# Kernel tuning notes

Hardware: AMD Instinct MI355X
Metric: run time of the kernel (lower is better)

The kernel has to match this reference:

```python
import jax, jax.numpy as jnp
import numpy as np

ATTN_K = 64
H = 256  # seq_hidden_size


def setup_inputs() -> dict:
    key = jax.random.key(0)
    ks = jax.random.split(key, 10)
    N, Q = 1000000, 256
    return {
        "question": jax.random.normal(ks[0], (Q,), jnp.float32),
        "score": jax.random.uniform(ks[1], (), jnp.float32),
        "questions": jax.random.normal(ks[2], (N, Q), jnp.float32),
        "hs": jax.random.normal(ks[3], (N, H), jnp.float32),
        "W_score": jax.random.normal(ks[4], (1, Q + H), jnp.float32) * 0.05,
        "b_score": jax.random.normal(ks[5], (1,), jnp.float32) * 0.05,
        "W_ih": jax.random.normal(ks[6], (3 * H, 2 * Q), jnp.float32) * 0.05,
        "W_hh": jax.random.normal(ks[7], (3 * H, H), jnp.float32) * 0.05,
        "b_ih": jax.random.normal(ks[8], (3 * H,), jnp.float32) * 0.05,
        "b_hh": jax.random.normal(ks[9], (3 * H,), jnp.float32) * 0.05,
    }


def reference(question, score, questions, hs, W_score, b_score, W_ih, W_hh, b_ih, b_hh):
    # Attention over history: dot-product scores, top-k, softmax-weighted sum.
    alpha = questions @ question                      # [N]
    vals, idx = jax.lax.top_k(alpha, ATTN_K)          # [k], [k]
    w = jax.nn.softmax(vals)                          # softmax over the k selected scores
    attn_h = w @ hs[idx]                              # [H] weighted gather-sum

    # Score head on [question ; attn_h]
    pred_v = jnp.concatenate([question, attn_h])      # [Q+H]
    pred = W_score @ pred_v + b_score                 # [1]

    # GRU input: question gated by correctness of score
    right = (score >= 0.5).astype(question.dtype)
    x = jnp.concatenate([question * right, question * (1.0 - right)])  # [2Q]

    # Single GRU step (PyTorch gate ordering: r, z, n)
    h = hs[-1]                                        # [H]
    gx = W_ih @ x + b_ih                              # [3H]
    gh = W_hh @ h + b_hh                              # [3H]
    xr, xz, xn = gx[:H], gx[H:2 * H], gx[2 * H:]
    hr, hz, hn = gh[:H], gh[H:2 * H], gh[2 * H:]
    r = jax.nn.sigmoid(xr + hr)
    z = jax.nn.sigmoid(xz + hz)
    n = jnp.tanh(xn + r * hn)
    h_new = (1.0 - z) * n + z * h                     # [H]
    return pred, h_new
```

## Files before the change

### kernel.cpp

```cpp
#include <hip/hip_runtime.h>
#include <math.h>

#define Q 256
#define H 256
#define ATTN_K 64
#define CAP 4096
#define HBINS 4096

typedef float f4 __attribute__((ext_vector_type(4)));

__device__ __forceinline__ unsigned f2k(float f) {
    unsigned u = __float_as_uint(f);
    return u ^ ((u & 0x80000000u) ? 0xFFFFFFFFu : 0x80000000u);
}

__global__ __launch_bounds__(256) void k_main(const float* __restrict__ questions,
                                              const float* __restrict__ question,
                                              const float* __restrict__ score,
                                              const float* __restrict__ hs,
                                              const float* __restrict__ W_ih,
                                              const float* __restrict__ W_hh,
                                              const float* __restrict__ b_ih,
                                              const float* __restrict__ b_hh,
                                              float* __restrict__ gx, float* __restrict__ gh,
                                              unsigned* __restrict__ hist,
                                              unsigned* __restrict__ state,
                                              float* __restrict__ alpha, int N) {
    const int t = threadIdx.x;
    const int b = blockIdx.x;
    if (b < 16) hist[b * 256 + t] = 0u;
    if (b == 16 && t < 16) state[t] = 0u;

    const int lane = t & 63;
    const int wid = b * 4 + (t >> 6);

    if (wid < 3 * H) {
        const int o = wid;
        const int off = (score[0] >= 0.5f) ? 0 : Q;
        const float4 q = *reinterpret_cast<const float4*>(question + lane * 4);
        const float4 h = *reinterpret_cast<const float4*>(hs + (size_t)(N - 1) * H + lane * 4);
        const float4 wx = *reinterpret_cast<const float4*>(W_ih + (size_t)o * (2 * Q) + off + lane * 4);
        const float4 wh = *reinterpret_cast<const float4*>(W_hh + (size_t)o * H + lane * 4);
        float px = wx.x * q.x + wx.y * q.y + wx.z * q.z + wx.w * q.w;
        float ph = wh.x * h.x + wh.y * h.y + wh.z * h.z + wh.w * h.w;
#pragma unroll
        for (int d = 32; d > 0; d >>= 1) {
            px += __shfl_xor(px, d, 64);
            ph += __shfl_xor(ph, d, 64);
        }
        if (lane == 0) {
            gx[o] = px + b_ih[o];
            gh[o] = ph + b_hh[o];
        }
    }

    const int sub = lane & 15;
    const int rg  = lane >> 4;
    const int nw  = (gridDim.x * blockDim.x) >> 6;

    float4 q[4];
#pragma unroll
    for (int j = 0; j < 4; ++j)
        q[j] = *reinterpret_cast<const float4*>(question + j * 64 + sub * 4);

    const size_t stepRows = (size_t)nw * 8;
    const float* baseA = questions + (size_t)(wid * 8 + rg) * Q + sub * 4;
    for (size_t r0 = (size_t)wid * 8; r0 < (size_t)N; r0 += stepRows, baseA += stepRows * Q) {
        const int rA = (int)r0 + rg;
        const int rB = rA + 4;
        float pA = 0.f, pB = 0.f;
        if (rA < N) {
#pragma unroll
            for (int j = 0; j < 4; ++j) {
                f4 x = __builtin_nontemporal_load(reinterpret_cast<const f4*>(baseA + j * 64));
                pA = fmaf(x.x, q[j].x, fmaf(x.y, q[j].y, fmaf(x.z, q[j].z, fmaf(x.w, q[j].w, pA))));
            }
        }
        if (rB < N) {
#pragma unroll
            for (int j = 0; j < 4; ++j) {
                f4 x = __builtin_nontemporal_load(reinterpret_cast<const f4*>(baseA + 4 * Q + j * 64));
                pB = fmaf(x.x, q[j].x, fmaf(x.y, q[j].y, fmaf(x.z, q[j].z, fmaf(x.w, q[j].w, pB))));
            }
        }
#pragma unroll
        for (int d = 1; d < 16; d <<= 1) {
            pA += __shfl_xor(pA, d, 64);
            pB += __shfl_xor(pB, d, 64);
        }
        if (sub == 0) {
            if (rA < N) alpha[rA] = pA;
            if (rB < N) alpha[rB] = pB;
        }
    }
}

__global__ __launch_bounds__(1024) void k_histscan(const float* __restrict__ alpha,
                                                   unsigned* __restrict__ hist,
                                                   unsigned* __restrict__ state, int N) {
    __shared__ unsigned hb[HBINS];
    __shared__ unsigned wsum[16];
    __shared__ int flag_sh;
    const int t = threadIdx.x;
#pragma unroll
    for (int j = 0; j < HBINS / 1024; ++j) hb[t + j * 1024] = 0u;
    __syncthreads();

    const int n4 = N >> 2;
    const int stride = gridDim.x * blockDim.x;
    const float4* a4 = reinterpret_cast<const float4*>(alpha);
    for (int i = blockIdx.x * blockDim.x + t; i < n4; i += stride) {
        float4 a = a4[i];
        float v[4] = {a.x, a.y, a.z, a.w};
#pragma unroll
        for (int j = 0; j < 4; ++j) {
            int rel = (int)(f2k(v[j]) >> 19) - 4096;
            if (rel >= 0) atomicAdd(&hb[rel], 1u);
        }
    }
    if (blockIdx.x == 0 && t < (N & 3)) {
        float v = alpha[(n4 << 2) + t];
        int rel = (int)(f2k(v) >> 19) - 4096;
        if (rel >= 0) atomicAdd(&hb[rel], 1u);
    }
    __syncthreads();
#pragma unroll
    for (int j = 0; j < HBINS / 1024; ++j) {
        unsigned v = hb[t + j * 1024];
        if (v) atomicAdd(&hist[t + j * 1024], v);
    }

    if (t == 0) {
        __threadfence();
        unsigned a = atomicAdd(&state[3], 1u);
        flag_sh = (a == gridDim.x - 1) ? 1 : 0;
    }
    __syncthreads();
    if (!flag_sh) return;
    __threadfence();

    const uint4* h4 = reinterpret_cast<const uint4*>(hist);
    uint4 hv = h4[1023 - t];
    unsigned x = hv.x + hv.y + hv.z + hv.w;

    const int lane = t & 63;
    const int w = t >> 6;
#pragma unroll
    for (int d = 1; d < 64; d <<= 1) {
        unsigned y = __shfl_up(x, d, 64);
        if (lane >= d) x += y;
    }
    if (lane == 63) wsum[w] = x;
    __syncthreads();
    if (w == 0 && lane < 16) {
        unsigned s = wsum[lane];
#pragma unroll
        for (int d = 1; d < 16; d <<= 1) {
            unsigned y = __shfl_up(s, d, 64);
            if (lane >= d) s += y;
        }
        wsum[lane] = s;
    }
    __syncthreads();
    unsigned cum = x + ((w > 0) ? wsum[w - 1] : 0u);
    hb[t] = cum;
    __syncthreads();
    if (cum >= (unsigned)ATTN_K && (t == 0 || hb[t - 1] < (unsigned)ATTN_K)) {
        const int s = t;
        unsigned acc = (s > 0) ? hb[s - 1] : 0u;
        const int hi = 4095 - 4 * s;
        int tb = hi - 3;
        for (int bin = hi; bin >= hi - 3; --bin) {
            acc += hist[bin];
            if (acc >= (unsigned)ATTN_K) { tb = bin; break; }
        }
        state[0] = (unsigned)(tb + 4096);
    }
}

__global__ __launch_bounds__(256) void k_collecthead(const float* __restrict__ alpha,
                                                     const float* __restrict__ question,
                                                     const float* __restrict__ hs,
                                                     const float* __restrict__ W_score,
                                                     const float* __restrict__ b_score,
                                                     unsigned* __restrict__ state,
                                                     float* __restrict__ cval, int* __restrict__ cidx,
                                                     const float* __restrict__ gx,
                                                     const float* __restrict__ gh,
                                                     float* __restrict__ out, int N) {
    __shared__ float lv[CAP];
    __shared__ int li[CAP];
    __shared__ float sw[ATTN_K];
    __shared__ int si[ATTN_K];
    __shared__ float red[256];
    __shared__ int flag_sh;
    const int t = threadIdx.x;
    const int tau = (int)state[0];

    {
        const int stride = gridDim.x * blockDim.x;
        const int n4 = N >> 2;
        const float4* a4 = reinterpret_cast<const float4*>(alpha);
        for (int i = blockIdx.x * blockDim.x + t; i < n4; i += stride) {
            float4 a = a4[i];
            float v[4] = {a.x, a.y, a.z, a.w};
#pragma unroll
            for (int j = 0; j < 4; ++j) {
                if ((int)(f2k(v[j]) >> 19) >= tau) {
                    unsigned p = atomicAdd(&state[1], 1u);
                    if (p < CAP) { cval[p] = v[j]; cidx[p] = i * 4 + j; }
                }
            }
        }
        if (blockIdx.x == 0 && t < (N & 3)) {
            const int idx = (n4 << 2) + t;
            float v = alpha[idx];
            if ((int)(f2k(v) >> 19) >= tau) {
                unsigned p = atomicAdd(&state[1], 1u);
                if (p < CAP) { cval[p] = v; cidx[p] = idx; }
            }
        }
    }

    if (t == 0) {
        __threadfence();
        unsigned a = atomicAdd(&state[2], 1u);
        flag_sh = (a == gridDim.x - 1) ? 1 : 0;
    }
    __syncthreads();
    if (!flag_sh) return;
    __threadfence();

    const int C = min((int)state[1], CAP);
    for (int i = t; i < C; i += 256) { lv[i] = cval[i]; li[i] = cidx[i]; }
    __syncthreads();

    if (t < 64) {
        for (int k = 0; k < ATTN_K; ++k) {
            float bv = -INFINITY;
            int bi = 0x7fffffff;
            int bp = -1;
            for (int i = t; i < C; i += 64) {
                float v = lv[i];
                int id = li[i];
                if (v > bv || (v == bv && id < bi)) { bv = v; bi = id; bp = i; }
            }
#pragma unroll
            for (int d = 32; d > 0; d >>= 1) {
                float ov = __shfl_xor(bv, d, 64);
                int oi = __shfl_xor(bi, d, 64);
                int op = __shfl_xor(bp, d, 64);
                if (ov > bv || (ov == bv && oi < bi)) { bv = ov; bi = oi; bp = op; }
            }
            if (t == 0) {
                sw[k] = bv;
                si[k] = (bi == 0x7fffffff) ? 0 : bi;
                if (bp >= 0) lv[bp] = -INFINITY;
            }
        }
        float m = sw[0];
        float e = expf(sw[t] - m);
        float ssum = e;
#pragma unroll
        for (int d = 32; d > 0; d >>= 1) ssum += __shfl_xor(ssum, d, 64);
        sw[t] = e / ssum;
    }
    __syncthreads();

    float aj = 0.f;
    for (int k = 0; k < ATTN_K; ++k) {
        aj = fmaf(sw[k], hs[(size_t)si[k] * H + t], aj);
    }

    red[t] = W_score[t] * question[t] + W_score[Q + t] * aj;
    __syncthreads();
    for (int d = 128; d > 0; d >>= 1) {
        if (t < d) red[t] += red[t + d];
        __syncthreads();
    }
    if (t == 0) out[0] = red[0] + b_score[0];

    {
        float xr = gx[t], xz = gx[H + t], xn = gx[2 * H + t];
        float hr = gh[t], hz = gh[H + t], hn = gh[2 * H + t];
        float r = 1.f / (1.f + expf(-(xr + hr)));
        float z = 1.f / (1.f + expf(-(xz + hz)));
        float n = tanhf(xn + r * hn);
        float hprev = hs[(size_t)(N - 1) * H + t];
        out[1 + t] = (1.f - z) * n + z * hprev;
    }
}

extern "C" void kernel_launch(void* const* d_in, const int* in_sizes, int n_in,
                              void* d_out, int out_size, void* d_ws, size_t ws_size,
                              hipStream_t stream) {
    const float* question = (const float*)d_in[0];
    const float* score    = (const float*)d_in[1];
    const float* questions= (const float*)d_in[2];
    const float* hs       = (const float*)d_in[3];
    const float* W_score  = (const float*)d_in[4];
    const float* b_score  = (const float*)d_in[5];
    const float* W_ih     = (const float*)d_in[6];
    const float* W_hh     = (const float*)d_in[7];
    const float* b_ih     = (const float*)d_in[8];
    const float* b_hh     = (const float*)d_in[9];
    const int N = in_sizes[2] / Q;
    float* out = (float*)d_out;

    char* ws = (char*)d_ws;
    size_t off = 0;
    float* alpha = (float*)(ws + off); off += (size_t)N * sizeof(float);
    off = (off + 255) & ~(size_t)255;
    unsigned* hist = (unsigned*)(ws + off); off += (size_t)HBINS * sizeof(unsigned);
    unsigned* state = (unsigned*)(ws + off); off += 256;
    float* cval = (float*)(ws + off); off += (size_t)CAP * sizeof(float);
    int* cidx = (int*)(ws + off); off += (size_t)CAP * sizeof(int);
    float* gx = (float*)(ws + off); off += 3 * H * sizeof(float);
    float* gh = (float*)(ws + off); off += 3 * H * sizeof(float);

    k_main<<<2048, 256, 0, stream>>>(questions, question, score, hs, W_ih, W_hh,
                                     b_ih, b_hh, gx, gh, hist, state, alpha, N);
    k_histscan<<<64, 1024, 0, stream>>>(alpha, hist, state, N);
    k_collecthead<<<512, 256, 0, stream>>>(alpha, question, hs, W_score, b_score,
                                           state, cval, cidx, gx, gh, out, N);
}
```

Baseline: 238.3 us.

## Fuse histogram, threshold scan and candidate collection into one kernel

Merges the histogram/scan kernel and the collect/head kernel into a single kernel. Each thread holds its alpha values in registers across both phases, and the phases are separated by a grid-wide spin wait on a sentinel threshold published with release/acquire atomics. This removes one launch and the second pass over alpha. The main dot-product loop also loses its per-row bounds checks through a separate tail loop, and the weighted gather-sum is spread across 1024 threads. The spin wait relies on all 256 large blocks being co-resident, which risks deadlock if occupancy does not allow that.

```diff
diff --git a/kernel.cpp b/kernel.cpp
--- a/kernel.cpp
+++ b/kernel.cpp
@@ -6,6 +6,9 @@
 #define ATTN_K 64
 #define CAP 4096
 #define HBINS 4096
+#define SENTINEL 0xFFFFFFFFu
+#define SEL_BLOCKS 256
+#define SEL_THREADS 1024
 
 typedef float f4 __attribute__((ext_vector_type(4)));
 
@@ -29,7 +32,7 @@
     const int t = threadIdx.x;
     const int b = blockIdx.x;
     if (b < 16) hist[b * 256 + t] = 0u;
-    if (b == 16 && t < 16) state[t] = 0u;
+    if (b == 16 && t < 16) state[t] = (t == 0) ? SENTINEL : 0u;
 
     const int lane = t & 63;
     const int wid = b * 4 + (t >> 6);
@@ -63,25 +66,20 @@
     for (int j = 0; j < 4; ++j)
         q[j] = *reinterpret_cast<const float4*>(question + j * 64 + sub * 4);
 
+    const int B = N / (nw * 8);
     const size_t stepRows = (size_t)nw * 8;
-    const float* baseA = questions + (size_t)(wid * 8 + rg) * Q + sub * 4;
-    for (size_t r0 = (size_t)wid * 8; r0 < (size_t)N; r0 += stepRows, baseA += stepRows * Q) {
-        const int rA = (int)r0 + rg;
-        const int rB = rA + 4;
+    const float* baseA = questions + ((size_t)wid * 8 + rg) * Q + sub * 4;
+    for (int it = 0; it < B; ++it, baseA += stepRows * Q) {
         float pA = 0.f, pB = 0.f;
-        if (rA < N) {
-#pragma unroll
-            for (int j = 0; j < 4; ++j) {
-                f4 x = __builtin_nontemporal_load(reinterpret_cast<const f4*>(baseA + j * 64));
-                pA = fmaf(x.x, q[j].x, fmaf(x.y, q[j].y, fmaf(x.z, q[j].z, fmaf(x.w, q[j].w, pA))));
-            }
-        }
-        if (rB < N) {
-#pragma unroll
-            for (int j = 0; j < 4; ++j) {
-                f4 x = __builtin_nontemporal_load(reinterpret_cast<const f4*>(baseA + 4 * Q + j * 64));
-                pB = fmaf(x.x, q[j].x, fmaf(x.y, q[j].y, fmaf(x.z, q[j].z, fmaf(x.w, q[j].w, pB))));
-            }
+#pragma unroll
+        for (int j = 0; j < 4; ++j) {
+            f4 x = __builtin_nontemporal_load(reinterpret_cast<const f4*>(baseA + j * 64));
+            pA = fmaf(x.x, q[j].x, fmaf(x.y, q[j].y, fmaf(x.z, q[j].z, fmaf(x.w, q[j].w, pA))));
+        }
+#pragma unroll
+        for (int j = 0; j < 4; ++j) {
+            f4 x = __builtin_nontemporal_load(reinterpret_cast<const f4*>(baseA + 4 * Q + j * 64));
+            pB = fmaf(x.x, q[j].x, fmaf(x.y, q[j].y, fmaf(x.z, q[j].z, fmaf(x.w, q[j].w, pB))));
         }
 #pragma unroll
         for (int d = 1; d < 16; d <<= 1) {
@@ -89,150 +87,162 @@
             pB += __shfl_xor(pB, d, 64);
         }
         if (sub == 0) {
-            if (rA < N) alpha[rA] = pA;
-            if (rB < N) alpha[rB] = pB;
-        }
+            const size_t r0 = (size_t)it * stepRows + (size_t)wid * 8 + rg;
+            alpha[r0] = pA;
+            alpha[r0 + 4] = pB;
+        }
+    }
+
+    const int tailStart = B * nw * 8;
+    for (int g = wid; tailStart + g * 4 < N; g += nw) {
+        const int r = tailStart + g * 4 + rg;
+        float p = 0.f;
+        if (r < N) {
+            const float* row = questions + (size_t)r * Q + sub * 4;
+#pragma unroll
+            for (int j = 0; j < 4; ++j) {
+                f4 x = __builtin_nontemporal_load(reinterpret_cast<const f4*>(row + j * 64));
+                p = fmaf(x.x, q[j].x, fmaf(x.y, q[j].y, fmaf(x.z, q[j].z, fmaf(x.w, q[j].w, p))));
+            }
+        }
+#pragma unroll
+        for (int d = 1; d < 16; d <<= 1) p += __shfl_xor(p, d, 64);
+        if (sub == 0 && r < N) alpha[r] = p;
     }
 }
 
-__global__ __launch_bounds__(1024) void k_histscan(const float* __restrict__ alpha,
-                                                   unsigned* __restrict__ hist,
-                                                   unsigned* __restrict__ state, int N) {
+__global__ __launch_bounds__(SEL_THREADS) void k_select(const float* __restrict__ alpha,
+                                                        const float* __restrict__ question,
+                                                        const float* __restrict__ hs,
+                                                        const float* __restrict__ W_score,
+                                                        const float* __restrict__ b_score,
+                                                        unsigned* __restrict__ hist,
+                                                        unsigned* __restrict__ state,
+                                                        float* __restrict__ cval,
+                                                        int* __restrict__ cidx,
+                                                        const float* __restrict__ gx,
+                                                        const float* __restrict__ gh,
+                                                        float* __restrict__ out, int N) {
     __shared__ unsigned hb[HBINS];
-    __shared__ unsigned wsum[16];
-    __shared__ int flag_sh;
-    const int t = threadIdx.x;
-#pragma unroll
-    for (int j = 0; j < HBINS / 1024; ++j) hb[t + j * 1024] = 0u;
-    __syncthreads();
-
-    const int n4 = N >> 2;
-    const int stride = gridDim.x * blockDim.x;
-    const float4* a4 = reinterpret_cast<const float4*>(alpha);
-    for (int i = blockIdx.x * blockDim.x + t; i < n4; i += stride) {
-        float4 a = a4[i];
-        float v[4] = {a.x, a.y, a.z, a.w};
-#pragma unroll
-        for (int j = 0; j < 4; ++j) {
-            int rel = (int)(f2k(v[j]) >> 19) - 4096;
-            if (rel >= 0) atomicAdd(&hb[rel], 1u);
-        }
-    }
-    if (blockIdx.x == 0 && t < (N & 3)) {
-        float v = alpha[(n4 << 2) + t];
-        int rel = (int)(f2k(v) >> 19) - 4096;
-        if (rel >= 0) atomicAdd(&hb[rel], 1u);
-    }
-    __syncthreads();
-#pragma unroll
-    for (int j = 0; j < HBINS / 1024; ++j) {
-        unsigned v = hb[t + j * 1024];
-        if (v) atomicAdd(&hist[t + j * 1024], v);
-    }
-
-    if (t == 0) {
-        __threadfence();
-        unsigned a = atomicAdd(&state[3], 1u);
-        flag_sh = (a == gridDim.x - 1) ? 1 : 0;
-    }
-    __syncthreads();
-    if (!flag_sh) return;
-    __threadfence();
-
-    const uint4* h4 = reinterpret_cast<const uint4*>(hist);
-    uint4 hv = h4[1023 - t];
-    unsigned x = hv.x + hv.y + hv.z + hv.w;
-
-    const int lane = t & 63;
-    const int w = t >> 6;
-#pragma unroll
-    for (int d = 1; d < 64; d <<= 1) {
-        unsigned y = __shfl_up(x, d, 64);
-        if (lane >= d) x += y;
-    }
-    if (lane == 63) wsum[w] = x;
-    __syncthreads();
-    if (w == 0 && lane < 16) {
-        unsigned s = wsum[lane];
-#pragma unroll
-        for (int d = 1; d < 16; d <<= 1) {
-            unsigned y = __shfl_up(s, d, 64);
-            if (lane >= d) s += y;
-        }
-        wsum[lane] = s;
-    }
-    __syncthreads();
-    unsigned cum = x + ((w > 0) ? wsum[w - 1] : 0u);
-    hb[t] = cum;
-    __syncthreads();
-    if (cum >= (unsigned)ATTN_K && (t == 0 || hb[t - 1] < (unsigned)ATTN_K)) {
-        const int s = t;
-        unsigned acc = (s > 0) ? hb[s - 1] : 0u;
-        const int hi = 4095 - 4 * s;
-        int tb = hi - 3;
-        for (int bin = hi; bin >= hi - 3; --bin) {
-            acc += hist[bin];
-            if (acc >= (unsigned)ATTN_K) { tb = bin; break; }
-        }
-        state[0] = (unsigned)(tb + 4096);
-    }
-}
-
-__global__ __launch_bounds__(256) void k_collecthead(const float* __restrict__ alpha,
-                                                     const float* __restrict__ question,
-                                                     const float* __restrict__ hs,
-                                                     const float* __restrict__ W_score,
-                                                     const float* __restrict__ b_score,
-                                                     unsigned* __restrict__ state,
-                                                     float* __restrict__ cval, int* __restrict__ cidx,
-                                                     const float* __restrict__ gx,
-                                                     const float* __restrict__ gh,
-                                                     float* __restrict__ out, int N) {
     __shared__ float lv[CAP];
     __shared__ int li[CAP];
+    __shared__ float apart[4][256];
     __shared__ float sw[ATTN_K];
     __shared__ int si[ATTN_K];
     __shared__ float red[256];
-    __shared__ int flag_sh;
+    __shared__ unsigned wsum[16];
+    __shared__ int last_sh;
+    __shared__ unsigned tau_sh;
     const int t = threadIdx.x;
-    const int tau = (int)state[0];
+    const int gid = blockIdx.x * SEL_THREADS + t;
+    const int n4 = N >> 2;
+    const int span = SEL_BLOCKS * SEL_THREADS;
+
+    for (int j = t; j < HBINS; j += SEL_THREADS) hb[j] = 0u;
+    __syncthreads();
+
+    const float4* a4 = reinterpret_cast<const float4*>(alpha);
+    float4 a0 = make_float4(-1.f, -1.f, -1.f, -1.f);
+    float4 a1 = make_float4(-1.f, -1.f, -1.f, -1.f);
+    if (gid < n4) a0 = a4[gid];
+    if (gid + span < n4) a1 = a4[gid + span];
+    float rem = -1.f;
+    if (blockIdx.x == 0 && t < (N & 3)) rem = alpha[(n4 << 2) + t];
 
     {
-        const int stride = gridDim.x * blockDim.x;
-        const int n4 = N >> 2;
-        const float4* a4 = reinterpret_cast<const float4*>(alpha);
-        for (int i = blockIdx.x * blockDim.x + t; i < n4; i += stride) {
-            float4 a = a4[i];
-            float v[4] = {a.x, a.y, a.z, a.w};
-#pragma unroll
-            for (int j = 0; j < 4; ++j) {
-                if ((int)(f2k(v[j]) >> 19) >= tau) {
-                    unsigned p = atomicAdd(&state[1], 1u);
-                    if (p < CAP) { cval[p] = v[j]; cidx[p] = i * 4 + j; }
-                }
-            }
-        }
-        if (blockIdx.x == 0 && t < (N & 3)) {
-            const int idx = (n4 << 2) + t;
-            float v = alpha[idx];
-            if ((int)(f2k(v) >> 19) >= tau) {
-                unsigned p = atomicAdd(&state[1], 1u);
-                if (p < CAP) { cval[p] = v; cidx[p] = idx; }
-            }
-        }
+        float v[9] = {a0.x, a0.y, a0.z, a0.w, a1.x, a1.y, a1.z, a1.w, rem};
+#pragma unroll
+        for (int j = 0; j < 9; ++j) {
+            int rel = (int)(f2k(v[j]) >> 19) - 4096;
+            if (rel >= 0) atomicAdd(&hb[rel], 1u);
+        }
+    }
+    __syncthreads();
+    for (int j = t; j < HBINS; j += SEL_THREADS) {
+        unsigned v = hb[j];
+        if (v) atomicAdd(&hist[j], v);
     }
 
     if (t == 0) {
         __threadfence();
-        unsigned a = atomicAdd(&state[2], 1u);
-        flag_sh = (a == gridDim.x - 1) ? 1 : 0;
-    }
-    __syncthreads();
-    if (!flag_sh) return;
+        last_sh = (atomicAdd(&state[2], 1u) == gridDim.x - 1) ? 1 : 0;
+    }
+    __syncthreads();
+    if (last_sh) {
+        __threadfence();
+        const uint4* h4 = reinterpret_cast<const uint4*>(hist);
+        uint4 hv = h4[1023 - t];
+        unsigned x = hv.x + hv.y + hv.z + hv.w;
+        const int lane = t & 63;
+        const int w = t >> 6;
+#pragma unroll
+        for (int d = 1; d < 64; d <<= 1) {
+            unsigned y = __shfl_up(x, d, 64);
+            if (lane >= d) x += y;
+        }
+        if (lane == 63) wsum[w] = x;
+        __syncthreads();
+        if (w == 0 && lane < 16) {
+            unsigned s = wsum[lane];
+#pragma unroll
+            for (int d = 1; d < 16; d <<= 1) {
+                unsigned y = __shfl_up(s, d, 64);
+                if (lane >= d) s += y;
+            }
+            wsum[lane] = s;
+        }
+        __syncthreads();
+        unsigned cum = x + ((w > 0) ? wsum[w - 1] : 0u);
+        hb[t] = cum;
+        __syncthreads();
+        if (cum >= (unsigned)ATTN_K && (t == 0 || hb[t - 1] < (unsigned)ATTN_K)) {
+            unsigned acc = (t > 0) ? hb[t - 1] : 0u;
+            const int hi = 4095 - 4 * t;
+            int tb = hi - 3;
+            for (int bin = hi; bin >= hi - 3; --bin) {
+                acc += hist[bin];
+                if (acc >= (unsigned)ATTN_K) { tb = bin; break; }
+            }
+            __hip_atomic_store(&state[0], (unsigned)(tb + 4096), __ATOMIC_RELEASE,
+                               __HIP_MEMORY_SCOPE_AGENT);
+        }
+    }
+
+    if (t == 0) {
+        unsigned tv;
+        while ((tv = __hip_atomic_load(&state[0], __ATOMIC_ACQUIRE,
+                                       __HIP_MEMORY_SCOPE_AGENT)) == SENTINEL)
+            __builtin_amdgcn_s_sleep(2);
+        tau_sh = tv;
+    }
+    __syncthreads();
+    const int tau = (int)tau_sh;
+
+    {
+        float v[9] = {a0.x, a0.y, a0.z, a0.w, a1.x, a1.y, a1.z, a1.w, rem};
+        int base0 = gid * 4, base1 = (gid + span) * 4;
+        int idxs[9] = {base0, base0 + 1, base0 + 2, base0 + 3,
+                       base1, base1 + 1, base1 + 2, base1 + 3,
+                       (n4 << 2) + t};
+#pragma unroll
+        for (int j = 0; j < 9; ++j) {
+            if ((int)(f2k(v[j]) >> 19) >= tau) {
+                unsigned p = atomicAdd(&state[1], 1u);
+                if (p < CAP) { cval[p] = v[j]; cidx[p] = idxs[j]; }
+            }
+        }
+    }
+
+    if (t == 0) {
+        __threadfence();
+        last_sh = (atomicAdd(&state[3], 1u) == gridDim.x - 1) ? 1 : 0;
+    }
+    __syncthreads();
+    if (!last_sh) return;
     __threadfence();
 
     const int C = min((int)state[1], CAP);
-    for (int i = t; i < C; i += 256) { lv[i] = cval[i]; li[i] = cidx[i]; }
+    for (int i = t; i < C; i += SEL_THREADS) { lv[i] = cval[i]; li[i] = cidx[i]; }
     __syncthreads();
 
     if (t < 64) {
@@ -267,12 +277,19 @@
     }
     __syncthreads();
 
-    float aj = 0.f;
-    for (int k = 0; k < ATTN_K; ++k) {
-        aj = fmaf(sw[k], hs[(size_t)si[k] * H + t], aj);
-    }
-
-    red[t] = W_score[t] * question[t] + W_score[Q + t] * aj;
+    {
+        const int qq = t >> 8;
+        const int j = t & 255;
+        float aj = 0.f;
+        for (int k = qq * 16; k < qq * 16 + 16; ++k)
+            aj = fmaf(sw[k], hs[(size_t)si[k] * H + j], aj);
+        apart[qq][j] = aj;
+    }
+    __syncthreads();
+    if (t < 256) {
+        float s = apart[0][t] + apart[1][t] + apart[2][t] + apart[3][t];
+        red[t] = W_score[t] * question[t] + W_score[Q + t] * s;
+    }
     __syncthreads();
     for (int d = 128; d > 0; d >>= 1) {
         if (t < d) red[t] += red[t + d];
@@ -280,7 +297,7 @@
     }
     if (t == 0) out[0] = red[0] + b_score[0];
 
-    {
+    if (t < 256) {
         float xr = gx[t], xz = gx[H + t], xn = gx[2 * H + t];
         float hr = gh[t], hz = gh[H + t], hn = gh[2 * H + t];
         float r = 1.f / (1.f + expf(-(xr + hr)));
@@ -320,7 +337,6 @@
 
     k_main<<<2048, 256, 0, stream>>>(questions, question, score, hs, W_ih, W_hh,
                                      b_ih, b_hh, gx, gh, hist, state, alpha, N);
-    k_histscan<<<64, 1024, 0, stream>>>(alpha, hist, state, N);
-    k_collecthead<<<512, 256, 0, stream>>>(alpha, question, hs, W_score, b_score,
-                                           state, cval, cidx, gx, gh, out, N);
+    k_select<<<SEL_BLOCKS, SEL_THREADS, 0, stream>>>(alpha, question, hs, W_score, b_score,
+                                                     hist, state, cval, cidx, gx, gh, out, N);
 }
```

Result: slower. 306.7 us (+28.7%).

## Fuse histogram into dot-product kernel and compute threshold redundantly per block

Applied to the files above, without the earlier changes.

Moves the alpha histogram build into the streaming dot-product kernel, using a per-block shared histogram flushed to 8 replicated global histograms. This removes the separate histscan pass that re-read alpha, along with its last-block scan. Each select block now merges the replicas and scans them itself to find the threshold bin. A small prep kernel takes over the GRU gate matvecs and the zeroing of the workspace. The cost is shared-memory atomics and an LDS footprint in the bandwidth-bound main kernel, plus redundant histogram reads in every select block.

```diff
diff --git a/kernel.cpp b/kernel.cpp
--- a/kernel.cpp
+++ b/kernel.cpp
@@ -6,6 +6,7 @@
 #define ATTN_K 64
 #define CAP 4096
 #define HBINS 4096
+#define NREP 8
 
 typedef float f4 __attribute__((ext_vector_type(4)));
 
@@ -14,8 +15,7 @@
     return u ^ ((u & 0x80000000u) ? 0xFFFFFFFFu : 0x80000000u);
 }
 
-__global__ __launch_bounds__(256) void k_main(const float* __restrict__ questions,
-                                              const float* __restrict__ question,
+__global__ __launch_bounds__(256) void k_prep(const float* __restrict__ question,
                                               const float* __restrict__ score,
                                               const float* __restrict__ hs,
                                               const float* __restrict__ W_ih,
@@ -24,38 +24,49 @@
                                               const float* __restrict__ b_hh,
                                               float* __restrict__ gx, float* __restrict__ gh,
                                               unsigned* __restrict__ hist,
-                                              unsigned* __restrict__ state,
-                                              float* __restrict__ alpha, int N) {
+                                              unsigned* __restrict__ state, int N) {
     const int t = threadIdx.x;
     const int b = blockIdx.x;
-    if (b < 16) hist[b * 256 + t] = 0u;
-    if (b == 16 && t < 16) state[t] = 0u;
+    const int gid = b * 256 + t;
+    if (gid < NREP * HBINS) hist[gid] = 0u;
+    if (gid < 16) state[gid] = 0u;
 
     const int lane = t & 63;
-    const int wid = b * 4 + (t >> 6);
-
-    if (wid < 3 * H) {
-        const int o = wid;
-        const int off = (score[0] >= 0.5f) ? 0 : Q;
-        const float4 q = *reinterpret_cast<const float4*>(question + lane * 4);
-        const float4 h = *reinterpret_cast<const float4*>(hs + (size_t)(N - 1) * H + lane * 4);
-        const float4 wx = *reinterpret_cast<const float4*>(W_ih + (size_t)o * (2 * Q) + off + lane * 4);
-        const float4 wh = *reinterpret_cast<const float4*>(W_hh + (size_t)o * H + lane * 4);
-        float px = wx.x * q.x + wx.y * q.y + wx.z * q.z + wx.w * q.w;
-        float ph = wh.x * h.x + wh.y * h.y + wh.z * h.z + wh.w * h.w;
-#pragma unroll
-        for (int d = 32; d > 0; d >>= 1) {
-            px += __shfl_xor(px, d, 64);
-            ph += __shfl_xor(ph, d, 64);
-        }
-        if (lane == 0) {
-            gx[o] = px + b_ih[o];
-            gh[o] = ph + b_hh[o];
-        }
-    }
-
+    const int o = b * 4 + (t >> 6);
+    if (o >= 3 * H) return;
+    const int off = (score[0] >= 0.5f) ? 0 : Q;
+    const float4 q = *reinterpret_cast<const float4*>(question + lane * 4);
+    const float4 h = *reinterpret_cast<const float4*>(hs + (size_t)(N - 1) * H + lane * 4);
+    const float4 wx = *reinterpret_cast<const float4*>(W_ih + (size_t)o * (2 * Q) + off + lane * 4);
+    const float4 wh = *reinterpret_cast<const float4*>(W_hh + (size_t)o * H + lane * 4);
+    float px = wx.x * q.x + wx.y * q.y + wx.z * q.z + wx.w * q.w;
+    float ph = wh.x * h.x + wh.y * h.y + wh.z * h.z + wh.w * h.w;
+#pragma unroll
+    for (int d = 32; d > 0; d >>= 1) {
+        px += __shfl_xor(px, d, 64);
+        ph += __shfl_xor(ph, d, 64);
+    }
+    if (lane == 0) {
+        gx[o] = px + b_ih[o];
+        gh[o] = ph + b_hh[o];
+    }
+}
+
+__global__ __launch_bounds__(256, 8) void k_main(const float* __restrict__ questions,
+                                                 const float* __restrict__ question,
+                                                 unsigned* __restrict__ hist,
+                                                 float* __restrict__ alpha, int N) {
+    __shared__ unsigned hb[HBINS];
+    const int t = threadIdx.x;
+    const int b = blockIdx.x;
+#pragma unroll
+    for (int j = 0; j < HBINS / 256; ++j) hb[t + j * 256] = 0u;
+    __syncthreads();
+
+    const int lane = t & 63;
     const int sub = lane & 15;
     const int rg  = lane >> 4;
+    const int wid = b * 4 + (t >> 6);
     const int nw  = (gridDim.x * blockDim.x) >> 6;
 
     float4 q[4];
@@ -64,7 +75,7 @@
         q[j] = *reinterpret_cast<const float4*>(question + j * 64 + sub * 4);
 
     const size_t stepRows = (size_t)nw * 8;
-    const float* baseA = questions + (size_t)(wid * 8 + rg) * Q + sub * 4;
+    const float* baseA = questions + ((size_t)wid * 8 + rg) * Q + sub * 4;
     for (size_t r0 = (size_t)wid * 8; r0 < (size_t)N; r0 += stepRows, baseA += stepRows * Q) {
         const int rA = (int)r0 + rg;
         const int rB = rA + 4;
@@ -89,124 +100,107 @@
             pB += __shfl_xor(pB, d, 64);
         }
         if (sub == 0) {
-            if (rA < N) alpha[rA] = pA;
-            if (rB < N) alpha[rB] = pB;
-        }
-    }
-}
-
-__global__ __launch_bounds__(1024) void k_histscan(const float* __restrict__ alpha,
-                                                   unsigned* __restrict__ hist,
-                                                   unsigned* __restrict__ state, int N) {
-    __shared__ unsigned hb[HBINS];
-    __shared__ unsigned wsum[16];
-    __shared__ int flag_sh;
-    const int t = threadIdx.x;
-#pragma unroll
-    for (int j = 0; j < HBINS / 1024; ++j) hb[t + j * 1024] = 0u;
-    __syncthreads();
-
-    const int n4 = N >> 2;
-    const int stride = gridDim.x * blockDim.x;
-    const float4* a4 = reinterpret_cast<const float4*>(alpha);
-    for (int i = blockIdx.x * blockDim.x + t; i < n4; i += stride) {
-        float4 a = a4[i];
-        float v[4] = {a.x, a.y, a.z, a.w};
-#pragma unroll
-        for (int j = 0; j < 4; ++j) {
-            int rel = (int)(f2k(v[j]) >> 19) - 4096;
-            if (rel >= 0) atomicAdd(&hb[rel], 1u);
-        }
-    }
-    if (blockIdx.x == 0 && t < (N & 3)) {
-        float v = alpha[(n4 << 2) + t];
-        int rel = (int)(f2k(v) >> 19) - 4096;
-        if (rel >= 0) atomicAdd(&hb[rel], 1u);
-    }
-    __syncthreads();
-#pragma unroll
-    for (int j = 0; j < HBINS / 1024; ++j) {
-        unsigned v = hb[t + j * 1024];
-        if (v) atomicAdd(&hist[t + j * 1024], v);
-    }
-
-    if (t == 0) {
-        __threadfence();
-        unsigned a = atomicAdd(&state[3], 1u);
-        flag_sh = (a == gridDim.x - 1) ? 1 : 0;
-    }
-    __syncthreads();
-    if (!flag_sh) return;
-    __threadfence();
-
-    const uint4* h4 = reinterpret_cast<const uint4*>(hist);
-    uint4 hv = h4[1023 - t];
-    unsigned x = hv.x + hv.y + hv.z + hv.w;
-
-    const int lane = t & 63;
-    const int w = t >> 6;
-#pragma unroll
-    for (int d = 1; d < 64; d <<= 1) {
-        unsigned y = __shfl_up(x, d, 64);
-        if (lane >= d) x += y;
-    }
-    if (lane == 63) wsum[w] = x;
-    __syncthreads();
-    if (w == 0 && lane < 16) {
-        unsigned s = wsum[lane];
-#pragma unroll
-        for (int d = 1; d < 16; d <<= 1) {
-            unsigned y = __shfl_up(s, d, 64);
-            if (lane >= d) s += y;
-        }
-        wsum[lane] = s;
-    }
-    __syncthreads();
-    unsigned cum = x + ((w > 0) ? wsum[w - 1] : 0u);
-    hb[t] = cum;
-    __syncthreads();
-    if (cum >= (unsigned)ATTN_K && (t == 0 || hb[t - 1] < (unsigned)ATTN_K)) {
-        const int s = t;
-        unsigned acc = (s > 0) ? hb[s - 1] : 0u;
-        const int hi = 4095 - 4 * s;
-        int tb = hi - 3;
-        for (int bin = hi; bin >= hi - 3; --bin) {
-            acc += hist[bin];
-            if (acc >= (unsigned)ATTN_K) { tb = bin; break; }
-        }
-        state[0] = (unsigned)(tb + 4096);
-    }
-}
-
-__global__ __launch_bounds__(256) void k_collecthead(const float* __restrict__ alpha,
-                                                     const float* __restrict__ question,
-                                                     const float* __restrict__ hs,
-                                                     const float* __restrict__ W_score,
-                                                     const float* __restrict__ b_score,
-                                                     unsigned* __restrict__ state,
-                                                     float* __restrict__ cval, int* __restrict__ cidx,
-                                                     const float* __restrict__ gx,
-                                                     const float* __restrict__ gh,
-                                                     float* __restrict__ out, int N) {
+            if (rA < N) {
+                alpha[rA] = pA;
+                int rel = (int)(f2k(pA) >> 19) - 4096;
+                if (rel >= 0) atomicAdd(&hb[rel], 1u);
+            }
+            if (rB < N) {
+                alpha[rB] = pB;
+                int rel = (int)(f2k(pB) >> 19) - 4096;
+                if (rel >= 0) atomicAdd(&hb[rel], 1u);
+            }
+        }
+    }
+
+    __syncthreads();
+    const unsigned rep = (unsigned)(b & (NREP - 1)) << 12;
+#pragma unroll
+    for (int j = 0; j < HBINS / 256; ++j) {
+        unsigned v = hb[t + j * 256];
+        if (v) atomicAdd(&hist[rep + t + j * 256], v);
+    }
+}
+
+__global__ __launch_bounds__(256) void k_select(const float* __restrict__ alpha,
+                                                const float* __restrict__ question,
+                                                const float* __restrict__ hs,
+                                                const float* __restrict__ W_score,
+                                                const float* __restrict__ b_score,
+                                                const unsigned* __restrict__ hist,
+                                                unsigned* __restrict__ state,
+                                                float* __restrict__ cval, int* __restrict__ cidx,
+                                                const float* __restrict__ gx,
+                                                const float* __restrict__ gh,
+                                                float* __restrict__ out, int N) {
     __shared__ float lv[CAP];
     __shared__ int li[CAP];
     __shared__ float sw[ATTN_K];
     __shared__ int si[ATTN_K];
     __shared__ float red[256];
-    __shared__ int flag_sh;
+    __shared__ unsigned wsum[4];
+    __shared__ int tau_sh;
+    __shared__ int last_sh;
     const int t = threadIdx.x;
-    const int tau = (int)state[0];
-
+    const int lane = t & 63;
+    const int w = t >> 6;
+
+    unsigned c[16];
     {
+        const int base16 = 4080 - 16 * t;
+#pragma unroll
+        for (int g = 0; g < 16; ++g) c[g] = 0u;
+#pragma unroll
+        for (int r = 0; r < NREP; ++r) {
+            const uint4* h4 = reinterpret_cast<const uint4*>(hist + (r << 12) + base16);
+#pragma unroll
+            for (int k = 0; k < 4; ++k) {
+                uint4 v = h4[k];
+                c[4 * k + 0] += v.x; c[4 * k + 1] += v.y;
+                c[4 * k + 2] += v.z; c[4 * k + 3] += v.w;
+            }
+        }
+    }
+    unsigned tsum = 0;
+#pragma unroll
+    for (int g = 0; g < 16; ++g) tsum += c[g];
+    unsigned cum = tsum;
+#pragma unroll
+    for (int d = 1; d < 64; d <<= 1) {
+        unsigned y = __shfl_up(cum, d, 64);
+        if (lane >= d) cum += y;
+    }
+    if (lane == 63) wsum[w] = cum;
+    __syncthreads();
+    {
+        unsigned add = 0;
+        for (int i = 0; i < w; ++i) add += wsum[i];
+        cum += add;
+    }
+    const unsigned before = cum - tsum;
+    if (cum >= (unsigned)ATTN_K && before < (unsigned)ATTN_K) {
+        unsigned acc = before;
+        int taub = 4080 - 16 * t;
+        for (int g = 15; g >= 0; --g) {
+            acc += c[g];
+            if (acc >= (unsigned)ATTN_K) { taub = 4080 - 16 * t + g; break; }
+        }
+        tau_sh = taub;
+    }
+    if (t == 255 && cum < (unsigned)ATTN_K) tau_sh = 0;
+    __syncthreads();
+    const int tau = tau_sh;
+
+    {
+        const int n4 = N >> 2;
         const int stride = gridDim.x * blockDim.x;
-        const int n4 = N >> 2;
         const float4* a4 = reinterpret_cast<const float4*>(alpha);
         for (int i = blockIdx.x * blockDim.x + t; i < n4; i += stride) {
             float4 a = a4[i];
             float v[4] = {a.x, a.y, a.z, a.w};
 #pragma unroll
             for (int j = 0; j < 4; ++j) {
-                if ((int)(f2k(v[j]) >> 19) >= tau) {
+                if ((int)(f2k(v[j]) >> 19) - 4096 >= tau) {
                     unsigned p = atomicAdd(&state[1], 1u);
                     if (p < CAP) { cval[p] = v[j]; cidx[p] = i * 4 + j; }
                 }
@@ -215,7 +209,7 @@
         if (blockIdx.x == 0 && t < (N & 3)) {
             const int idx = (n4 << 2) + t;
             float v = alpha[idx];
-            if ((int)(f2k(v) >> 19) >= tau) {
+            if ((int)(f2k(v) >> 19) - 4096 >= tau) {
                 unsigned p = atomicAdd(&state[1], 1u);
                 if (p < CAP) { cval[p] = v; cidx[p] = idx; }
             }
@@ -224,11 +218,10 @@
 
     if (t == 0) {
         __threadfence();
-        unsigned a = atomicAdd(&state[2], 1u);
-        flag_sh = (a == gridDim.x - 1) ? 1 : 0;
-    }
-    __syncthreads();
-    if (!flag_sh) return;
+        last_sh = (atomicAdd(&state[2], 1u) == gridDim.x - 1) ? 1 : 0;
+    }
+    __syncthreads();
+    if (!last_sh) return;
     __threadfence();
 
     const int C = min((int)state[1], CAP);
@@ -311,16 +304,16 @@
     size_t off = 0;
     float* alpha = (float*)(ws + off); off += (size_t)N * sizeof(float);
     off = (off + 255) & ~(size_t)255;
-    unsigned* hist = (unsigned*)(ws + off); off += (size_t)HBINS * sizeof(unsigned);
+    unsigned* hist = (unsigned*)(ws + off); off += (size_t)NREP * HBINS * sizeof(unsigned);
     unsigned* state = (unsigned*)(ws + off); off += 256;
     float* cval = (float*)(ws + off); off += (size_t)CAP * sizeof(float);
     int* cidx = (int*)(ws + off); off += (size_t)CAP * sizeof(int);
     float* gx = (float*)(ws + off); off += 3 * H * sizeof(float);
     float* gh = (float*)(ws + off); off += 3 * H * sizeof(float);
 
-    k_main<<<2048, 256, 0, stream>>>(questions, question, score, hs, W_ih, W_hh,
-                                     b_ih, b_hh, gx, gh, hist, state, alpha, N);
-    k_histscan<<<64, 1024, 0, stream>>>(alpha, hist, state, N);
-    k_collecthead<<<512, 256, 0, stream>>>(alpha, question, hs, W_score, b_score,
-                                           state, cval, cidx, gx, gh, out, N);
-}
+    k_prep<<<192, 256, 0, stream>>>(question, score, hs, W_ih, W_hh, b_ih, b_hh,
+                                    gx, gh, hist, state, N);
+    k_main<<<2048, 256, 0, stream>>>(questions, question, hist, alpha, N);
+    k_select<<<512, 256, 0, stream>>>(alpha, question, hs, W_score, b_score, hist,
+                                      state, cval, cidx, gx, gh, out, N);
+}
```

Result: slower. 243.3 us (+2.1%).
